# Kernel optimization log

Hardware: AMD Instinct MI355X
Metric: run time of the kernel (lower is better)

The kernel has to match this reference:

```python
import jax, jax.numpy as jnp
import numpy as np

NEG_INF = -9e15
ALPHA = 0.2  # LeakyReLU negative slope
OUT_FEATURES = 128


def setup_inputs() -> dict:
    key = jax.random.key(0)
    k1, k2, k3, k4 = jax.random.split(key, 4)
    B, N, F_in, F_out = 4, 4096, 256, OUT_FEATURES
    h = jax.random.normal(k1, (B, N, F_in), dtype=jnp.float32)
    adj = jax.random.randint(k2, (B, N, N), 0, 2, dtype=jnp.int32)
    W = jax.random.normal(k3, (F_in, F_out), dtype=jnp.float32) * 0.07
    a = jax.random.normal(k4, (2 * F_out, 1), dtype=jnp.float32) * 0.1
    return {"h": h, "adj": adj, "W": W, "a": a}


def reference(h, adj, W, a):
    # Wh: (B, N, F_out)
    Wh = jnp.einsum('bni,io->bno', h, W)
    a1 = a[:OUT_FEATURES, 0]   # (F_out,)
    a2 = a[OUT_FEATURES:, 0]   # (F_out,)
    Wh1 = Wh @ a1              # (B, N)
    Wh2 = Wh @ a2              # (B, N)
    e = Wh1[:, :, None] + Wh2[:, None, :]          # (B, N, N)
    e = jnp.where(e >= 0, e, ALPHA * e)             # LeakyReLU
    e = jnp.where(adj > 0, e, NEG_INF)              # adjacency mask
    attention = jax.nn.softmax(e, axis=-1)          # (B, N, N)
    # dropout omitted: reference runs in eval mode (training=False)
    h_prime = jnp.einsum('bnm,bmo->bno', attention, Wh)
    return jax.nn.elu(h_prime)  # concat=True
```

## Files before the change

kernel.cpp:

```cpp
#include <hip/hip_runtime.h>
#include <hip/hip_bf16.h>
#include <math.h>

typedef __attribute__((ext_vector_type(4))) float  f32x4;
typedef __attribute__((ext_vector_type(4))) int    i32x4;
typedef __attribute__((ext_vector_type(8))) short  s16x8;
typedef __attribute__((ext_vector_type(4))) short  s16x4;
typedef __attribute__((ext_vector_type(8))) __bf16 bf16x8;

#define LOG2E 1.4426950408889634f

__device__ __forceinline__ short f32_to_bf16_rne(float f) {
    unsigned u = __builtin_bit_cast(unsigned, f);
    u += 0x7fffu + ((u >> 16) & 1u);
    return (short)(u >> 16);
}
__device__ __forceinline__ int pack2_bf16(float f0, float f1) {
    unsigned u0 = __builtin_bit_cast(unsigned, f0) + 0x8000u;
    unsigned u1 = __builtin_bit_cast(unsigned, f1) + 0x8000u;
    return (int)((u0 >> 16) | (u1 & 0xffff0000u));
}
__device__ __forceinline__ bf16x8 as_bf16x8(s16x8 v) {
    return __builtin_bit_cast(bf16x8, v);
}
__device__ __forceinline__ bf16x8 as_bf16x8(i32x4 v) {
    return __builtin_bit_cast(bf16x8, v);
}

__global__ void k0_wt(const float* __restrict__ W, short* __restrict__ WT) {
    int g = blockIdx.x * 256 + threadIdx.x;
    int col = g >> 6;
    int k0 = (g & 63) * 4;
    s16x4 v;
    #pragma unroll
    for (int i = 0; i < 4; ++i) v[i] = f32_to_bf16_rne(W[(k0 + i) * 128 + col]);
    *(s16x4*)(WT + col * 256 + k0) = v;
}

__global__ __launch_bounds__(256, 2) void k1_gemm(
    const float* __restrict__ h, const float* __restrict__ a,
    const short* __restrict__ WT,
    short* __restrict__ WhT, float* __restrict__ Wh1p, float* __restrict__ Tp)
{
    int l = threadIdx.x & 63;
    int w = threadIdx.x >> 6;
    int gw = blockIdx.x * 4 + w;
    int r0 = gw * 16;
    int lm = l & 15, q = l >> 4;

    f32x4 acc[8];
    #pragma unroll
    for (int ct = 0; ct < 8; ++ct) acc[ct] = (f32x4)0.0f;

    const float* hrow = h + (long)(r0 + lm) * 256;
    for (int kb = 0; kb < 8; ++kb) {
        int kbase = kb * 32 + q * 8;
        f32x4 h0 = *(const f32x4*)(hrow + kbase);
        f32x4 h1 = *(const f32x4*)(hrow + kbase + 4);
        s16x8 af;
        #pragma unroll
        for (int j = 0; j < 4; ++j) af[j] = f32_to_bf16_rne(h0[j]);
        #pragma unroll
        for (int j = 0; j < 4; ++j) af[4 + j] = f32_to_bf16_rne(h1[j]);
        bf16x8 afb = as_bf16x8(af);
        #pragma unroll
        for (int ct = 0; ct < 8; ++ct) {
            s16x8 bf = *(const s16x8*)(WT + (ct * 16 + lm) * 256 + kbase);
            acc[ct] = __builtin_amdgcn_mfma_f32_16x16x32_bf16(afb, as_bf16x8(bf), acc[ct], 0, 0, 0);
        }
    }

    int b = r0 >> 12;
    int nb = r0 & 4095;
    float p1[4] = {0.f, 0.f, 0.f, 0.f}, p2[4] = {0.f, 0.f, 0.f, 0.f};
    #pragma unroll
    for (int ct = 0; ct < 8; ++ct) {
        int col = ct * 16 + lm;
        float a1c = a[col], a2c = a[128 + col];
        s16x4 vv;
        #pragma unroll
        for (int r = 0; r < 4; ++r) {
            float v = acc[ct][r];
            p1[r] += v * a1c;
            p2[r] += v * a2c;
            vv[r] = f32_to_bf16_rne(v);
        }
        *(s16x4*)(WhT + ((long)(b * 128 + col) * 4096 + nb + q * 4)) = vv;
    }
    #pragma unroll
    for (int off = 1; off < 16; off <<= 1) {
        #pragma unroll
        for (int r = 0; r < 4; ++r) {
            p1[r] += __shfl_xor(p1[r], off);
            p2[r] += __shfl_xor(p2[r], off);
        }
    }
    if (lm == 0) {
        #pragma unroll
        for (int r = 0; r < 4; ++r) {
            int row = r0 + q * 4 + r;
            Wh1p[row] = LOG2E * p1[r];
            Tp[row]   = LOG2E * p2[r];
        }
    }
}

__global__ void k2_tmax(const float* __restrict__ Tp, float* __restrict__ Tmax) {
    __shared__ float red[256];
    int b = blockIdx.x, t = threadIdx.x;
    float mx = -1e30f;
    for (int i = 0; i < 16; ++i) mx = fmaxf(mx, Tp[b * 4096 + t + i * 256]);
    red[t] = mx;
    __syncthreads();
    for (int s = 128; s > 0; s >>= 1) {
        if (t < s) red[t] = fmaxf(red[t], red[t + s]);
        __syncthreads();
    }
    if (t == 0) Tmax[b] = red[0];
}

template <int SPLIT>
__global__ __launch_bounds__(256, 2) void k3_attn(
    const int* __restrict__ adj, const short* __restrict__ WhT,
    const float* __restrict__ Wh1p, const float* __restrict__ Tp,
    const float* __restrict__ Tmax,
    float* __restrict__ U, float* __restrict__ Z)
{
    const int MSLICE = 4096 / SPLIT;
    const int MTILES = MSLICE / 128;
    __shared__ __align__(16) short tile[2][128 * 128];
    __shared__ __align__(16) float tps[4096 / SPLIT];

    int l = threadIdx.x & 63, w = threadIdx.x >> 6;
    int lm = l & 15, q = l >> 4;
    int bid = blockIdx.x;
    int mh = bid & (SPLIT - 1);
    int rg = (bid / SPLIT) & 63;
    int b  = bid / (SPLIT * 64);
    int n0 = rg * 64;
    int mbase = mh * MSLICE;

    int n_lane = n0 + w * 16 + lm;
    float sp = Wh1p[b * 4096 + n_lane];
    float xm = sp + Tmax[b];
    float Mrow = fmaxf(xm, 0.2f * xm);

    const int*   adjrow = adj + ((long)(b * 4096 + n_lane) << 12) + q * 8;
    const short* whtb   = WhT + (long)b * 128 * 4096;
    const float* tpsq   = tps + q * 8;

    {
        const float* tg = Tp + b * 4096 + mbase;
        int i0 = threadIdx.x * 4;
        *(f32x4*)(tps + i0)        = *(const f32x4*)(tg + i0);
        *(f32x4*)(tps + i0 + 1024) = *(const f32x4*)(tg + i0 + 1024);
    }

    f32x4 acc[8];
    #pragma unroll
    for (int ct = 0; ct < 8; ++ct) acc[ct] = (f32x4)0.0f;
    float z = 0.0f;

    auto stage = [&](short* dst, int m0) {
        int colw = w * 32;
        #pragma unroll
        for (int j = 0; j < 8; ++j) {
            int cb = colw + j * 4;
            int col = cb + q;
            int gch = lm ^ (col & 7);
            const short* gp = whtb + (long)col * 4096 + m0 + gch * 8;
            __builtin_amdgcn_global_load_lds(
                (const __attribute__((address_space(1))) void*)gp,
                (__attribute__((address_space(3))) void*)(dst + cb * 128), 16, 0, 0);
        }
    };
    auto ldadj = [&](i32x4* aj, int m0) {
        #pragma unroll
        for (int ks = 0; ks < 4; ++ks) {
            aj[2 * ks]     = *(const i32x4*)(adjrow + m0 + ks * 32);
            aj[2 * ks + 1] = *(const i32x4*)(adjrow + m0 + ks * 32 + 4);
        }
    };
    auto compute = [&](const short* buf, const i32x4* aj, int mrel) {
        #pragma unroll
        for (int ks = 0; ks < 4; ++ks) {
            f32x4 t0 = *(const f32x4*)(tpsq + mrel + ks * 32);
            f32x4 t1 = *(const f32x4*)(tpsq + mrel + ks * 32 + 4);
            i32x4 pk;
            float zs = 0.0f;
            #pragma unroll
            for (int half = 0; half < 2; ++half) {
                i32x4 a4 = aj[2 * ks + half];
                f32x4 t4 = half ? t1 : t0;
                float wv[4];
                #pragma unroll
                for (int j = 0; j < 4; ++j) {
                    float y = sp + t4[j];
                    float e = fmaxf(y, 0.2f * y) - Mrow;
                    float v = __builtin_amdgcn_exp2f(e);
                    v = (a4[j] != 0) ? v : 0.0f;
                    zs += v; wv[j] = v;
                }
                pk[half * 2]     = pack2_bf16(wv[0], wv[1]);
                pk[half * 2 + 1] = pack2_bf16(wv[2], wv[3]);
            }
            z += zs;
            bf16x8 ab = as_bf16x8(pk);
            #pragma unroll
            for (int ct = 0; ct < 8; ++ct) {
                int col = ct * 16 + lm;
                int pos = (ks * 4 + q) ^ (col & 7);
                s16x8 bf = *(const s16x8*)(buf + col * 128 + pos * 8);
                acc[ct] = __builtin_amdgcn_mfma_f32_16x16x32_bf16(ab, as_bf16x8(bf), acc[ct], 0, 0, 0);
            }
        }
    };

    i32x4 ajA[8], ajB[8];
    stage(tile[0], mbase);
    ldadj(ajA, mbase);
    __syncthreads();

    #pragma unroll 1
    for (int t = 0; t < MTILES; t += 2) {
        int r1 = (t + 1) & (MTILES - 1);
        stage(tile[1], mbase + r1 * 128);
        ldadj(ajB, mbase + r1 * 128);
        __builtin_amdgcn_sched_barrier(0);
        compute(tile[0], ajA, t * 128);
        __syncthreads();
        int r2 = (t + 2) & (MTILES - 1);
        stage(tile[0], mbase + r2 * 128);
        ldadj(ajA, mbase + r2 * 128);
        __builtin_amdgcn_sched_barrier(0);
        compute(tile[1], ajB, r1 * 128);
        __syncthreads();
    }

    z += __shfl_xor(z, 16);
    z += __shfl_xor(z, 32);

    int slice = b * SPLIT + mh;
    if (l < 16) Z[slice * 4096 + n0 + w * 16 + lm] = z;
    float* ub = U + ((long)slice * 4096 + n0 + w * 16) * 128;
    #pragma unroll
    for (int ct = 0; ct < 8; ++ct) {
        int col = ct * 16 + lm;
        #pragma unroll
        for (int r = 0; r < 4; ++r)
            ub[(q * 4 + r) * 128 + col] = acc[ct][r];
    }
}

__global__ void k4_combine(const float* __restrict__ U, const float* __restrict__ Z,
                           float* __restrict__ out) {
    long g = (long)blockIdx.x * 256 + threadIdx.x;
    long off = g * 4;
    long nf = off >> 7;
    int b = (int)(nf >> 12), n = (int)(nf & 4095), col = (int)(off & 127);
    long base0 = ((long)(b * 2) * 4096 + n) * 128 + col;
    f32x4 u0 = *(const f32x4*)(U + base0);
    f32x4 u1 = *(const f32x4*)(U + base0 + (long)4096 * 128);
    float zz = Z[(b * 2) * 4096 + n] + Z[(b * 2 + 1) * 4096 + n];
    f32x4 v;
    #pragma unroll
    for (int i = 0; i < 4; ++i) {
        float x = (u0[i] + u1[i]) / zz;
        v[i] = (x > 0.f) ? x : (expf(x) - 1.0f);
    }
    *(f32x4*)(out + off) = v;
}

extern "C" void kernel_launch(void* const* d_in, const int* in_sizes, int n_in,
                              void* d_out, int out_size, void* d_ws, size_t ws_size,
                              hipStream_t stream) {
    const float* h   = (const float*)d_in[0];
    const int*   adj = (const int*)d_in[1];
    const float* W   = (const float*)d_in[2];
    const float* a   = (const float*)d_in[3];
    float* out = (float*)d_out;

    char* ws = (char*)d_ws;
    short* WhT  = (short*)ws;
    short* WT   = (short*)(ws + 4194304);
    float* Wh1p = (float*)(ws + 4259840);
    float* Tp   = (float*)(ws + 4325376);
    float* Tmax = (float*)(ws + 4390912);
    float* U    = (float*)(ws + 4391168);
    float* Z    = (float*)(ws + 4391168 + 16777216);

    k0_wt<<<32, 256, 0, stream>>>(W, WT);
    k1_gemm<<<256, 256, 0, stream>>>(h, a, WT, WhT, Wh1p, Tp);
    k2_tmax<<<4, 256, 0, stream>>>(Tp, Tmax);
    k3_attn<2><<<512, 256, 0, stream>>>(adj, WhT, Wh1p, Tp, Tmax, U, Z);
    k4_combine<<<2048, 256, 0, stream>>>(U, Z, out);
    (void)in_sizes; (void)n_in; (void)out_size; (void)ws_size;
}
```

Measured before the change: 405.3 us.

## Pack adjacency into bitmask in a pre-pass and remap attention block order

Adds a kernel that compresses the int32 adjacency matrix into 32-bit bitmasks. The attention kernel then reads one 16-byte word of bits per tile instead of many int vectors, which cuts its adjacency traffic and register pressure. The full adjacency is still read once by the pack kernel, and the bits make an extra write and read round trip through memory. Block indexing is also remapped so that batch and slice vary fastest across neighbouring blocks.

```diff
diff --git a/kernel.cpp b/kernel.cpp
--- a/kernel.cpp
+++ b/kernel.cpp
@@ -25,6 +25,20 @@
 }
 __device__ __forceinline__ bf16x8 as_bf16x8(i32x4 v) {
     return __builtin_bit_cast(bf16x8, v);
+}
+
+__global__ void k_pack(const int* __restrict__ adj, unsigned* __restrict__ bits) {
+    long g = (long)blockIdx.x * 256 + threadIdx.x;
+    const int* p = adj + g * 32;
+    unsigned r = 0;
+    #pragma unroll
+    for (int c = 0; c < 8; ++c) {
+        i32x4 v = *(const i32x4*)(p + c * 4);
+        #pragma unroll
+        for (int j = 0; j < 4; ++j)
+            r |= (v[j] > 0) ? (1u << (c * 4 + j)) : 0u;
+    }
+    bits[g] = r;
 }
 
 __global__ void k0_wt(const float* __restrict__ W, short* __restrict__ WT) {
@@ -121,7 +135,7 @@
 
 template <int SPLIT>
 __global__ __launch_bounds__(256, 2) void k3_attn(
-    const int* __restrict__ adj, const short* __restrict__ WhT,
+    const unsigned* __restrict__ bits, const short* __restrict__ WhT,
     const float* __restrict__ Wh1p, const float* __restrict__ Tp,
     const float* __restrict__ Tmax,
     float* __restrict__ U, float* __restrict__ Z)
@@ -134,9 +148,10 @@
     int l = threadIdx.x & 63, w = threadIdx.x >> 6;
     int lm = l & 15, q = l >> 4;
     int bid = blockIdx.x;
-    int mh = bid & (SPLIT - 1);
-    int rg = (bid / SPLIT) & 63;
-    int b  = bid / (SPLIT * 64);
+    int p8 = bid & 7;
+    int b  = p8 >> 1;
+    int mh = p8 & 1;
+    int rg = bid >> 3;
     int n0 = rg * 64;
     int mbase = mh * MSLICE;
 
@@ -145,9 +160,9 @@
     float xm = sp + Tmax[b];
     float Mrow = fmaxf(xm, 0.2f * xm);
 
-    const int*   adjrow = adj + ((long)(b * 4096 + n_lane) << 12) + q * 8;
-    const short* whtb   = WhT + (long)b * 128 * 4096;
-    const float* tpsq   = tps + q * 8;
+    const unsigned* bitrow = bits + (long)(b * 4096 + n_lane) * 128;
+    const short* whtb = WhT + (long)b * 128 * 4096;
+    const float* tpsq = tps + q * 8;
 
     {
         const float* tg = Tp + b * 4096 + mbase;
@@ -174,31 +189,25 @@
                 (__attribute__((address_space(3))) void*)(dst + cb * 128), 16, 0, 0);
         }
     };
-    auto ldadj = [&](i32x4* aj, int m0) {
-        #pragma unroll
-        for (int ks = 0; ks < 4; ++ks) {
-            aj[2 * ks]     = *(const i32x4*)(adjrow + m0 + ks * 32);
-            aj[2 * ks + 1] = *(const i32x4*)(adjrow + m0 + ks * 32 + 4);
-        }
-    };
-    auto compute = [&](const short* buf, const i32x4* aj, int mrel) {
+    auto compute = [&](const short* buf, const i32x4 bv, int mrel) {
         #pragma unroll
         for (int ks = 0; ks < 4; ++ks) {
             f32x4 t0 = *(const f32x4*)(tpsq + mrel + ks * 32);
             f32x4 t1 = *(const f32x4*)(tpsq + mrel + ks * 32 + 4);
+            unsigned wb = ((unsigned)bv[ks]) >> (q * 8);
             i32x4 pk;
             float zs = 0.0f;
             #pragma unroll
             for (int half = 0; half < 2; ++half) {
-                i32x4 a4 = aj[2 * ks + half];
                 f32x4 t4 = half ? t1 : t0;
+                unsigned nib = wb >> (half * 4);
                 float wv[4];
                 #pragma unroll
                 for (int j = 0; j < 4; ++j) {
                     float y = sp + t4[j];
                     float e = fmaxf(y, 0.2f * y) - Mrow;
                     float v = __builtin_amdgcn_exp2f(e);
-                    v = (a4[j] != 0) ? v : 0.0f;
+                    v = (nib & (1u << j)) ? v : 0.0f;
                     zs += v; wv[j] = v;
                 }
                 pk[half * 2]     = pack2_bf16(wv[0], wv[1]);
@@ -216,24 +225,24 @@
         }
     };
 
-    i32x4 ajA[8], ajB[8];
+    i32x4 bvA, bvB;
     stage(tile[0], mbase);
-    ldadj(ajA, mbase);
+    bvA = *(const i32x4*)(bitrow + (mbase >> 5));
     __syncthreads();
 
     #pragma unroll 1
     for (int t = 0; t < MTILES; t += 2) {
         int r1 = (t + 1) & (MTILES - 1);
         stage(tile[1], mbase + r1 * 128);
-        ldadj(ajB, mbase + r1 * 128);
+        bvB = *(const i32x4*)(bitrow + ((mbase + r1 * 128) >> 5));
         __builtin_amdgcn_sched_barrier(0);
-        compute(tile[0], ajA, t * 128);
+        compute(tile[0], bvA, t * 128);
         __syncthreads();
         int r2 = (t + 2) & (MTILES - 1);
         stage(tile[0], mbase + r2 * 128);
-        ldadj(ajA, mbase + r2 * 128);
+        bvA = *(const i32x4*)(bitrow + ((mbase + r2 * 128) >> 5));
         __builtin_amdgcn_sched_barrier(0);
-        compute(tile[1], ajB, r1 * 128);
+        compute(tile[1], bvB, r1 * 128);
         __syncthreads();
     }
 
@@ -288,11 +297,13 @@
     float* Tmax = (float*)(ws + 4390912);
     float* U    = (float*)(ws + 4391168);
     float* Z    = (float*)(ws + 4391168 + 16777216);
-
+    unsigned* bits = (unsigned*)(ws + 21299200);
+
+    k_pack<<<8192, 256, 0, stream>>>(adj, bits);
     k0_wt<<<32, 256, 0, stream>>>(W, WT);
     k1_gemm<<<256, 256, 0, stream>>>(h, a, WT, WhT, Wh1p, Tp);
     k2_tmax<<<4, 256, 0, stream>>>(Tp, Tmax);
-    k3_attn<2><<<512, 256, 0, stream>>>(adj, WhT, Wh1p, Tp, Tmax, U, Z);
+    k3_attn<2><<<512, 256, 0, stream>>>(bits, WhT, Wh1p, Tp, Tmax, U, Z);
     k4_combine<<<2048, 256, 0, stream>>>(U, Z, out);
     (void)in_sizes; (void)n_in; (void)out_size; (void)ws_size;
 }
```

Result: slower. 437.8 us (+8.0%).

## Deepen adjacency prefetch to two tiles ahead and remap block order

Applied to the files above, without the earlier changes.

The main loop now keeps four register buffers of adjacency data so adj loads for tile t+2 are issued while tile t computes. Shared-memory staging stays one tile ahead. Explicit s_waitcnt with a vmcnt threshold and raw s_barrier replace __syncthreads, so outstanding adj loads stay in flight across the barrier. Block indexing is also changed so that consecutive blocks cover different batches and m-slices of the same row group, which alters L2 locality. The extra register buffers raise VGPR pressure. The hand-picked vmcnt count must match the number of loads issued by stage and ldadj, or the code can read data that has not arrived.

```diff
diff --git a/kernel.cpp b/kernel.cpp
--- a/kernel.cpp
+++ b/kernel.cpp
@@ -134,9 +134,10 @@
     int l = threadIdx.x & 63, w = threadIdx.x >> 6;
     int lm = l & 15, q = l >> 4;
     int bid = blockIdx.x;
-    int mh = bid & (SPLIT - 1);
-    int rg = (bid / SPLIT) & 63;
-    int b  = bid / (SPLIT * 64);
+    int p8 = bid & (4 * SPLIT - 1);
+    int b  = p8 / SPLIT;
+    int mh = p8 % SPLIT;
+    int rg = bid / (4 * SPLIT);
     int n0 = rg * 64;
     int mbase = mh * MSLICE;
 
@@ -216,26 +217,37 @@
         }
     };
 
-    i32x4 ajA[8], ajB[8];
+    #define SUBPHASE(CBUF, SBUF, AJ_LD, AJ_USE, TC, TS, TA)                    \
+        stage(SBUF, mbase + ((TS) & (MTILES - 1)) * 128);                      \
+        __builtin_amdgcn_sched_barrier(0);                                     \
+        ldadj(AJ_LD, mbase + ((TA) & (MTILES - 1)) * 128);                     \
+        __builtin_amdgcn_sched_barrier(0);                                     \
+        asm volatile("s_waitcnt vmcnt(24)" ::: "memory");                      \
+        __builtin_amdgcn_s_barrier();                                          \
+        __builtin_amdgcn_sched_barrier(0);                                     \
+        compute(CBUF, AJ_USE, (TC) * 128);                                     \
+        __builtin_amdgcn_sched_barrier(0);                                     \
+        __builtin_amdgcn_s_barrier();                                          \
+        __builtin_amdgcn_sched_barrier(0);
+
+    i32x4 ajA[8], ajB[8], ajC[8], ajD[8];
     stage(tile[0], mbase);
+    __builtin_amdgcn_sched_barrier(0);
     ldadj(ajA, mbase);
-    __syncthreads();
+    ldadj(ajB, mbase + 128);
+    __builtin_amdgcn_sched_barrier(0);
+    asm volatile("s_waitcnt vmcnt(0) lgkmcnt(0)" ::: "memory");
+    __builtin_amdgcn_s_barrier();
+    __builtin_amdgcn_sched_barrier(0);
 
     #pragma unroll 1
-    for (int t = 0; t < MTILES; t += 2) {
-        int r1 = (t + 1) & (MTILES - 1);
-        stage(tile[1], mbase + r1 * 128);
-        ldadj(ajB, mbase + r1 * 128);
-        __builtin_amdgcn_sched_barrier(0);
-        compute(tile[0], ajA, t * 128);
-        __syncthreads();
-        int r2 = (t + 2) & (MTILES - 1);
-        stage(tile[0], mbase + r2 * 128);
-        ldadj(ajA, mbase + r2 * 128);
-        __builtin_amdgcn_sched_barrier(0);
-        compute(tile[1], ajB, r1 * 128);
-        __syncthreads();
-    }
+    for (int t = 0; t < MTILES; t += 4) {
+        SUBPHASE(tile[0], tile[1], ajC, ajA, t,     t + 1, t + 2)
+        SUBPHASE(tile[1], tile[0], ajD, ajB, t + 1, t + 2, t + 3)
+        SUBPHASE(tile[0], tile[1], ajA, ajC, t + 2, t + 3, t + 4)
+        SUBPHASE(tile[1], tile[0], ajB, ajD, t + 3, t + 4, t + 5)
+    }
+    #undef SUBPHASE
 
     z += __shfl_xor(z, 16);
     z += __shfl_xor(z, 32);
```

New measurement: 415.5 us. +2.5%, slower.
